# Optimization experiments

Measured on AMD Instinct MI355X. Metric: run time of the kernel, lower is better.

## Reference

```python
import jax, jax.numpy as jnp
import numpy as np


def _forward(x, wc, we, Wb1, bb1, Wb2, bb2, Wr1, br1, Wr2, br2,
             Wq1, bq1, Wq2, bq2, Wq3, bq3, Wo1, bo1, Wo2, bo2, Wo3, bo3, scale):
    bs, c, h, w = x.shape
    Hs, Ws = scale * h, scale * w
    fh = (jnp.arange(Hs, dtype=jnp.float32) + 0.5) / scale
    fw = (jnp.arange(Ws, dtype=jnp.float32) + 0.5) / scale
    coor_h = fh - jnp.floor(fh + 0.001) - 0.5  # [Hs] fractional phase
    coor_w = fw - jnp.floor(fw + 0.001) - 0.5  # [Ws]
    ones_hw = jnp.ones((Hs, Ws), jnp.float32)
    meta = jnp.stack([ones_hw, ones_hw / scale,
                      jnp.broadcast_to(coor_h[:, None], (Hs, Ws)),
                      jnp.broadcast_to(coor_w[None, :], (Hs, Ws))], 0)  # [4,Hs,Ws]
    chan_mean = x.mean(axis=(0, 2, 3))  # [c]
    chan_scale = jnp.concatenate([chan_mean[:, None], jnp.ones((c, 3), jnp.float32)], axis=1)  # [c,4]
    inp = meta[None] * chan_scale[:, :, None, None]  # [c,4,Hs,Ws]

    # body: 1x1x1 Conv3d over spectral-channel axis c
    lin = lambda W, b, t: jnp.einsum('oc,cfhw->ofhw', W, t) + b[:, None, None, None]
    emb = jax.nn.relu(lin(Wb2, bb2, jax.nn.relu(lin(Wb1, bb1, inp))))  # [c,4,Hs,Ws]

    # offset head: Conv2d 1x1 with batch = c, features = 4 -> 2
    lin2 = lambda W, b, t: jnp.einsum('of,cfhw->cohw', W, t) + b[None, :, None, None]
    off = lin2(Wo3, bo3, jax.nn.relu(lin2(Wo2, bo2, jax.nn.relu(lin2(Wo1, bo1, emb)))))  # [c,2,Hs,Ws]

    # routing_1: Conv3d over c -> 1 channel, sigmoid
    r = jax.nn.sigmoid(lin(Wr2, br2, jax.nn.relu(lin(Wr1, br1, emb))))[0]  # [4,Hs,Ws]
    # routing_2: Conv2d 1x1 over the 4 meta-features -> E experts
    lin3 = lambda W, b, t: jnp.einsum('of,fhw->ohw', W, t) + b[:, None, None]
    rw = jax.nn.sigmoid(lin3(Wq3, bq3, jax.nn.relu(lin3(Wq2, bq2, jax.nn.relu(lin3(Wq1, bq1, r))))))  # [E,Hs,Ws]

    # per-channel offset grid_sample (bilinear, zeros padding, align_corners=True)
    px0 = fw - 0.5  # [Ws] base source x coord
    py0 = fh - 0.5  # [Hs]

    def sample(img, offx, offy):  # img [bs,h,w]; off* [Hs,Ws]
        px = px0[None, :] + offx
        py = py0[:, None] + offy
        x0 = jnp.floor(px); y0 = jnp.floor(py)
        wx = px - x0; wy = py - y0
        x0i = x0.astype(jnp.int32); y0i = y0.astype(jnp.int32)
        def g(yi, xi):
            v = ((xi >= 0) & (xi <= w - 1) & (yi >= 0) & (yi <= h - 1)).astype(img.dtype)
            return img[:, jnp.clip(yi, 0, h - 1), jnp.clip(xi, 0, w - 1)] * v[None]
        return (g(y0i, x0i) * ((1 - wy) * (1 - wx))[None]
                + g(y0i, x0i + 1) * ((1 - wy) * wx)[None]
                + g(y0i + 1, x0i) * (wy * (1 - wx))[None]
                + g(y0i + 1, x0i + 1) * (wy * wx)[None])

    fea0 = jax.vmap(lambda xi, oi: sample(xi, oi[0], oi[1]),
                    in_axes=(1, 0), out_axes=1)(x, off)  # [bs,c,Hs,Ws]

    # per-pixel expert-mixed compress/expand: (sum_e r_e Wc_e) f then (sum_e r_e We_e)
    mid = jnp.einsum('ehw,ekc,bchw->bkhw', rw, wc, fea0)   # [bs,c//8,Hs,Ws]
    out = jnp.einsum('ehw,eck,bkhw->bchw', rw, we, mid)    # [bs,c,Hs,Ws]
    return out + fea0


def setup_inputs() -> dict:
    key = jax.random.key(0)
    ks = jax.random.split(key, 32)
    bs, c, h, w = 4, 64, 64, 64
    E, k = 4, c // 8
    s = 0.05
    d = {
        'x': jax.random.normal(ks[0], (bs, c, h, w), jnp.float32),
        'wc': jax.random.normal(ks[1], (E, k, c), jnp.float32) * s,
        'we': jax.random.normal(ks[2], (E, c, k), jnp.float32) * s,
        'Wb1': jax.random.normal(ks[3], (c, c), jnp.float32) * s,
        'bb1': jax.random.normal(ks[4], (c,), jnp.float32) * s,
        'Wb2': jax.random.normal(ks[5], (c, c), jnp.float32) * s,
        'bb2': jax.random.normal(ks[6], (c,), jnp.float32) * s,
        'Wr1': jax.random.normal(ks[7], (64, c), jnp.float32) * s,
        'br1': jax.random.normal(ks[8], (64,), jnp.float32) * s,
        'Wr2': jax.random.normal(ks[9], (1, 64), jnp.float32) * s,
        'br2': jax.random.normal(ks[10], (1,), jnp.float32) * s,
        'Wq1': jax.random.normal(ks[11], (64, 4), jnp.float32) * s,
        'bq1': jax.random.normal(ks[12], (64,), jnp.float32) * s,
        'Wq2': jax.random.normal(ks[13], (64, 64), jnp.float32) * s,
        'bq2': jax.random.normal(ks[14], (64,), jnp.float32) * s,
        'Wq3': jax.random.normal(ks[15], (E, 64), jnp.float32) * s,
        'bq3': jax.random.normal(ks[16], (E,), jnp.float32) * s,
        'Wo1': jax.random.normal(ks[17], (64, 4), jnp.float32) * s,
        'bo1': jax.random.normal(ks[18], (64,), jnp.float32) * s,
        'Wo2': jax.random.normal(ks[19], (64, 64), jnp.float32) * s,
        'bo2': jax.random.normal(ks[20], (64,), jnp.float32) * s,
        'Wo3': jax.random.normal(ks[21], (2, 64), jnp.float32) * s,
        'bo3': jax.random.normal(ks[22], (2,), jnp.float32) * s,
        'scale': 4,
    }
    return d


def reference(x, wc, we, Wb1, bb1, Wb2, bb2, Wr1, br1, Wr2, br2,
              Wq1, bq1, Wq2, bq2, Wq3, bq3, Wo1, bo1, Wo2, bo2, Wo3, bo3, scale):
    return _forward(x, wc, we, Wb1, bb1, Wb2, bb2, Wr1, br1, Wr2, br2,
                    Wq1, bq1, Wq2, bq2, Wq3, bq3, Wo1, bo1, Wo2, bo2, Wo3, bo3, int(scale))
```

## Files before the change

kernel.cpp:

```cpp
#include <hip/hip_runtime.h>


__device__ __forceinline__ float relu_(float v){ return fmaxf(v, 0.f); }
__device__ __forceinline__ float sigm_(float v){ return 1.f/(1.f + __expf(-v)); }

__global__ void k_mean(const float* __restrict__ x, float* __restrict__ ws) {
  const int ch = blockIdx.x, b = blockIdx.y, t = threadIdx.x;
  const float4* p = reinterpret_cast<const float4*>(x + (size_t)(b*64 + ch)*4096);
  float4 v0 = p[t], v1 = p[t+256], v2 = p[t+512], v3 = p[t+768];
  float s = ((v0.x+v0.y)+(v0.z+v0.w)) + ((v1.x+v1.y)+(v1.z+v1.w))
          + ((v2.x+v2.y)+(v2.z+v2.w)) + ((v3.x+v3.y)+(v3.z+v3.w));
  __shared__ float red[256];
  red[t] = s; __syncthreads();
  for (int off = 128; off > 0; off >>= 1) {
    if (t < off) red[t] += red[t + off];
    __syncthreads();
  }
  if (t == 0) ws[18496 + b*64 + ch] = red[0];
}

__launch_bounds__(256)
__global__ void k_phase(const float* __restrict__ wc, const float* __restrict__ we,
    const float* __restrict__ Wb1, const float* __restrict__ bb1,
    const float* __restrict__ Wb2, const float* __restrict__ bb2,
    const float* __restrict__ Wr1, const float* __restrict__ br1,
    const float* __restrict__ Wr2, const float* __restrict__ br2,
    const float* __restrict__ Wq1, const float* __restrict__ bq1,
    const float* __restrict__ Wq2, const float* __restrict__ bq2,
    const float* __restrict__ Wq3, const float* __restrict__ bq3,
    const float* __restrict__ Wo1, const float* __restrict__ bo1,
    const float* __restrict__ Wo2, const float* __restrict__ bo2,
    const float* __restrict__ Wo3, const float* __restrict__ bo3,
    float* __restrict__ ws)
{
  const int p = blockIdx.x, pi = p >> 2, pj = p & 3;
  const int t = threadIdx.x;
  const float chv = 0.25f*pi - 0.375f, cwv = 0.25f*pj - 0.375f;

  __shared__ float WbL1[64*66];
  __shared__ float WbL2[64*66];
  __shared__ float WrL1[64*66];
  __shared__ float WqL2[64*66];
  __shared__ __align__(16) float Wo2L[4096];
  __shared__ __align__(16) float Wo1L[256];
  __shared__ __align__(16) float wcL[2048];
  __shared__ __align__(16) float weL[2048];
  __shared__ float Wo3L[128];
  __shared__ float Wq1L[256], Wq3L[256];
  __shared__ float Wr2L[64];
  __shared__ float bb1L[64], bb2L[64], br1L[64], bq1L[64], bq2L[64];
  __shared__ float bo1L[64], bo2L[64];

  __shared__ float meanL[64];
  __shared__ __align__(16) float t1L[64][4];
  __shared__ __align__(16) float embL[64][4];
  __shared__ __align__(16) float rpL[64][4];
  __shared__ float r4[4];
  __shared__ float q1L[64], q2L[64];
  __shared__ float rwL[4];
  __shared__ float oxL[64][4], oyL[64][4];

  {
    const float* srcs[4] = {Wb1, Wb2, Wr1, Wq2};
    float* dsts[4] = {WbL1, WbL2, WrL1, WqL2};
    for (int m = 0; m < 4; ++m) {
      const float4* W4 = reinterpret_cast<const float4*>(srcs[m]);
      float* WL = dsts[m];
      for (int v = t; v < 1024; v += 256) {
        float4 d = W4[v];
        const int r = v >> 4, c = (v & 15) << 2;
        float* q = &WL[r*66 + c];
        q[0] = d.x; q[1] = d.y; q[2] = d.z; q[3] = d.w;
      }
    }
    for (int v = t; v < 1024; v += 256)
      reinterpret_cast<float4*>(Wo2L)[v] = reinterpret_cast<const float4*>(Wo2)[v];
    for (int v = t; v < 512; v += 256) {
      reinterpret_cast<float4*>(wcL)[v] = reinterpret_cast<const float4*>(wc)[v];
      reinterpret_cast<float4*>(weL)[v] = reinterpret_cast<const float4*>(we)[v];
    }
    if (t < 64) {
      reinterpret_cast<float4*>(Wo1L)[t] = reinterpret_cast<const float4*>(Wo1)[t];
      reinterpret_cast<float4*>(Wq1L)[t] = reinterpret_cast<const float4*>(Wq1)[t];
      reinterpret_cast<float4*>(Wq3L)[t] = reinterpret_cast<const float4*>(Wq3)[t];
      bb1L[t] = bb1[t]; bb2L[t] = bb2[t]; br1L[t] = br1[t];
      bq1L[t] = bq1[t]; bq2L[t] = bq2[t];
      bo1L[t] = bo1[t]; bo2L[t] = bo2[t];
      Wr2L[t] = Wr2[t];
      const float* wsp = ws + 18496;
      meanL[t] = (wsp[t] + wsp[64+t] + wsp[128+t] + wsp[192+t]) * (1.f/16384.f);
    }
    if (t >= 64 && t < 192) Wo3L[t-64] = Wo3[t-64];
  }
  __syncthreads();

  if (t < 64) {
    float a0 = 0.f, as = 0.f;
    const float* row = &WbL1[t*66];
    #pragma unroll 8
    for (int c = 0; c < 64; ++c) { float w = row[c]; a0 += w*meanL[c]; as += w; }
    float bb = bb1L[t];
    t1L[t][0] = relu_(a0 + bb);
    t1L[t][1] = relu_(0.25f*as + bb);
    t1L[t][2] = relu_(chv*as + bb);
    t1L[t][3] = relu_(cwv*as + bb);
  }
  __syncthreads();
  if (t < 64) {
    float bb = bb2L[t];
    float e0=bb,e1=bb,e2=bb,e3=bb;
    const float* row = &WbL2[t*66];
    #pragma unroll 8
    for (int c = 0; c < 64; ++c) {
      float w = row[c];
      float4 tv = *reinterpret_cast<const float4*>(&t1L[c][0]);
      e0 += w*tv.x; e1 += w*tv.y; e2 += w*tv.z; e3 += w*tv.w;
    }
    embL[t][0]=relu_(e0); embL[t][1]=relu_(e1); embL[t][2]=relu_(e2); embL[t][3]=relu_(e3);
  }
  __syncthreads();
  if (t < 64) {
    float bb = br1L[t];
    float p0=bb,p1=bb,p2=bb,p3=bb;
    const float* row = &WrL1[t*66];
    #pragma unroll 8
    for (int c = 0; c < 64; ++c) {
      float w = row[c];
      float4 ev = *reinterpret_cast<const float4*>(&embL[c][0]);
      p0 += w*ev.x; p1 += w*ev.y; p2 += w*ev.z; p3 += w*ev.w;
    }
    rpL[t][0]=relu_(p0); rpL[t][1]=relu_(p1); rpL[t][2]=relu_(p2); rpL[t][3]=relu_(p3);
  }
  __syncthreads();
  if (t < 4) {
    float acc = br2[0];
    #pragma unroll 8
    for (int c = 0; c < 64; ++c) acc += Wr2L[c]*rpL[c][t];
    r4[t] = sigm_(acc);
  }
  __syncthreads();
  if (t < 64) {
    float acc = bq1L[t];
    #pragma unroll
    for (int f = 0; f < 4; ++f) acc += Wq1L[t*4+f]*r4[f];
    q1L[t] = relu_(acc);
  }
  __syncthreads();
  if (t < 64) {
    float acc = bq2L[t];
    const float* row = &WqL2[t*66];
    #pragma unroll 8
    for (int c = 0; c < 64; ++c) acc += row[c]*q1L[c];
    q2L[t] = relu_(acc);
  }
  __syncthreads();
  if (t < 4) {
    float acc = bq3[t];
    #pragma unroll 8
    for (int c = 0; c < 64; ++c) acc += Wq3L[t*64+c]*q2L[c];
    rwL[t] = sigm_(acc);
  }
  __syncthreads();

  {
    const int ch = t & 63, q = t >> 6;
    const float4 e = *reinterpret_cast<const float4*>(&embL[ch][0]);
    float v1[64];
    #pragma unroll
    for (int o = 0; o < 64; ++o) {
      float4 w = *reinterpret_cast<const float4*>(&Wo1L[o*4]);
      v1[o] = relu_(w.x*e.x + w.y*e.y + w.z*e.z + w.w*e.w + bo1L[o]);
    }
    float ox = 0.f, oy = 0.f;
    for (int o = q*16; o < q*16+16; ++o) {
      float acc = bo2L[o];
      const float4* row = reinterpret_cast<const float4*>(&Wo2L[o*64]);
      #pragma unroll
      for (int k = 0; k < 16; ++k) {
        float4 w = row[k];
        acc += w.x*v1[4*k+0] + w.y*v1[4*k+1] + w.z*v1[4*k+2] + w.w*v1[4*k+3];
      }
      acc = relu_(acc);
      ox += Wo3L[o]*acc;
      oy += Wo3L[64+o]*acc;
    }
    oxL[ch][q] = ox; oyL[ch][q] = oy;
  }
  __syncthreads();

  float* ws_off = ws + 64;
  float* ws_wcT = ws + 2112;
  float* ws_weT = ws + 10304;
  if (t < 64) {
    ws_off[(p*64+t)*2+0] = oxL[t][0]+oxL[t][1]+oxL[t][2]+oxL[t][3] + bo3[0];
    ws_off[(p*64+t)*2+1] = oyL[t][0]+oyL[t][1]+oyL[t][2]+oyL[t][3] + bo3[1];
  }
  const float r0 = rwL[0], r1 = rwL[1], r2 = rwL[2], r3 = rwL[3];
  for (int idx = t; idx < 512; idx += 256) {
    const int ch = idx >> 3, k = idx & 7;
    ws_wcT[p*512 + idx] = r0*wcL[(0*8+k)*64+ch] + r1*wcL[(1*8+k)*64+ch]
                        + r2*wcL[(2*8+k)*64+ch] + r3*wcL[(3*8+k)*64+ch];
    ws_weT[p*512 + idx] = r0*weL[(0*64+ch)*8+k] + r1*weL[(1*64+ch)*8+k]
                        + r2*weL[(2*64+ch)*8+k] + r3*weL[(3*64+ch)*8+k];
  }
}

__launch_bounds__(256, 3)
__global__ void k_main(const float* __restrict__ x, const float* __restrict__ ws,
                       float* __restrict__ out) {
  const int i = blockIdx.x;
  const int b = blockIdx.y;
  const int j = threadIdx.x;
  const int pi = i & 3;
  const int pj = j & 3;

  __shared__ float wcT[4*520];
  __shared__ float weT[4*520];
  __shared__ float offxL[4*68];
  __shared__ int4  rowi[256];

  const float* wsoff = ws + 64;
  const float* wswc  = ws + 2112;
  const float* wswe  = ws + 10304;

  for (int idx = threadIdx.x; idx < 2048; idx += 256) {
    const int ph = idx >> 9, rem = idx & 511;
    wcT[ph*520 + rem] = wswc[(pi*4 + ph)*512 + rem];
    weT[ph*520 + rem] = wswe[(pi*4 + ph)*512 + rem];
  }
  {
    const int ch = threadIdx.x >> 2, ph = threadIdx.x & 3;
    const int p = pi*4 + ph;
    const float ox = wsoff[(p*64 + ch)*2 + 0];
    const float oy = wsoff[(p*64 + ch)*2 + 1];
    offxL[ph*68 + ch] = ox;
    const float py = i*0.25f - 0.375f + oy;
    const float fy = floorf(py);
    const float wy = py - fy;
    const int y0 = (int)fy, y1 = y0 + 1;
    const int y0c = min(max(y0, 0), 63), y1c = min(max(y1, 0), 63);
    const float wy0 = ((unsigned)y0 <= 63u) ? (1.f - wy) : 0.f;
    const float wy1 = ((unsigned)y1 <= 63u) ? wy : 0.f;
    rowi[ch*4 + ph] = make_int4(ch*4096 + y0c*64, ch*4096 + y1c*64,
                                __float_as_int(wy0), __float_as_int(wy1));
  }
  __syncthreads();

  const float* __restrict__ xb = x + (size_t)b*64*4096;
  const float px0 = j*0.25f - 0.375f;

  float fea[64];
  float mid[8] = {0.f,0.f,0.f,0.f,0.f,0.f,0.f,0.f};

  const float4* wc_pj = reinterpret_cast<const float4*>(&wcT[pj*520]);
  const float* offx_pj = &offxL[pj*68];
  const int4* rowi_pj = &rowi[pj];

  #pragma unroll
  for (int ch = 0; ch < 64; ++ch) {
    const int4 ri = rowi_pj[ch*4];
    const float px = px0 + offx_pj[ch];
    const float fx = floorf(px);
    const float wx = px - fx;
    const int x0 = (int)fx, x1 = x0 + 1;
    const int x0c = min(max(x0, 0), 63), x1c = min(max(x1, 0), 63);
    const float wx0 = ((unsigned)x0 <= 63u) ? (1.f - wx) : 0.f;
    const float wx1 = ((unsigned)x1 <= 63u) ? wx : 0.f;
    const float g00 = xb[ri.x + x0c], g01 = xb[ri.x + x1c];
    const float g10 = xb[ri.y + x0c], g11 = xb[ri.y + x1c];
    const float f0 = g00*wx0 + g01*wx1;
    const float f1 = g10*wx0 + g11*wx1;
    const float fv = f0*__int_as_float(ri.z) + f1*__int_as_float(ri.w);
    fea[ch] = fv;
    const float4 wa = wc_pj[ch*2], wb = wc_pj[ch*2+1];
    mid[0] += wa.x*fv; mid[1] += wa.y*fv; mid[2] += wa.z*fv; mid[3] += wa.w*fv;
    mid[4] += wb.x*fv; mid[5] += wb.y*fv; mid[6] += wb.z*fv; mid[7] += wb.w*fv;
  }

  const float4* we_pj = reinterpret_cast<const float4*>(&weT[pj*520]);
  float* op = out + (size_t)(b*64)*65536 + i*256 + j;
  #pragma unroll
  for (int ch = 0; ch < 64; ++ch) {
    const float4 wa = we_pj[ch*2], wb = we_pj[ch*2+1];
    float acc = fea[ch];
    acc += wa.x*mid[0] + wa.y*mid[1] + wa.z*mid[2] + wa.w*mid[3];
    acc += wb.x*mid[4] + wb.y*mid[5] + wb.z*mid[6] + wb.w*mid[7];
    op[ch*65536] = acc;
  }
}

extern "C" void kernel_launch(void* const* d_in, const int* in_sizes, int n_in,
                              void* d_out, int out_size, void* d_ws, size_t ws_size,
                              hipStream_t stream) {
  const float* x   = (const float*)d_in[0];
  const float* wc  = (const float*)d_in[1];
  const float* we  = (const float*)d_in[2];
  const float* Wb1 = (const float*)d_in[3];
  const float* bb1 = (const float*)d_in[4];
  const float* Wb2 = (const float*)d_in[5];
  const float* bb2 = (const float*)d_in[6];
  const float* Wr1 = (const float*)d_in[7];
  const float* br1 = (const float*)d_in[8];
  const float* Wr2 = (const float*)d_in[9];
  const float* br2 = (const float*)d_in[10];
  const float* Wq1 = (const float*)d_in[11];
  const float* bq1 = (const float*)d_in[12];
  const float* Wq2 = (const float*)d_in[13];
  const float* bq2 = (const float*)d_in[14];
  const float* Wq3 = (const float*)d_in[15];
  const float* bq3 = (const float*)d_in[16];
  const float* Wo1 = (const float*)d_in[17];
  const float* bo1 = (const float*)d_in[18];
  const float* Wo2 = (const float*)d_in[19];
  const float* bo2 = (const float*)d_in[20];
  const float* Wo3 = (const float*)d_in[21];
  const float* bo3 = (const float*)d_in[22];
  float* ws  = (float*)d_ws;
  float* out = (float*)d_out;

  k_mean<<<dim3(64, 4), 256, 0, stream>>>(x, ws);
  k_phase<<<16, 256, 0, stream>>>(wc, we, Wb1, bb1, Wb2, bb2, Wr1, br1, Wr2, br2,
                                  Wq1, bq1, Wq2, bq2, Wq3, bq3,
                                  Wo1, bo1, Wo2, bo2, Wo3, bo3, ws);
  k_main<<<dim3(256, 4), 256, 0, stream>>>(x, ws, out);
}
```

Before: 163.6 us.

## Remap main kernel so each wavefront owns one phase and reads precomputed tables

The phase kernel now precomputes per-(phase, channel) x-offset parameters, packed interleaved wc/we mixing weights, and full per-row y-index/weight tables into workspace. The main kernel drops its shared-memory staging and barrier, assigns one column phase per wavefront so mixing weights and offsets are wave-uniform scalar loads, and raises launch bounds occupancy to 4. This removes per-block LDS setup and redundant y-coordinate math, but writes output with a stride-4 interleaved column pattern and adds a large y-table in global memory.

New measurement: 197.7 us. 20.8% more time.

```diff
diff --git a/kernel.cpp b/kernel.cpp
--- a/kernel.cpp
+++ b/kernel.cpp
@@ -16,7 +16,7 @@
     if (t < off) red[t] += red[t + off];
     __syncthreads();
   }
-  if (t == 0) ws[18496 + b*64 + ch] = red[0];
+  if (t == 0) ws[b*64 + ch] = red[0];
 }
 
 __launch_bounds__(256)
@@ -59,6 +59,7 @@
   __shared__ float q1L[64], q2L[64];
   __shared__ float rwL[4];
   __shared__ float oxL[64][4], oyL[64][4];
+  __shared__ float oxF[64], oyF[64];
 
   {
     const float* srcs[4] = {Wb1, Wb2, Wr1, Wq2};
@@ -87,7 +88,7 @@
       bq1L[t] = bq1[t]; bq2L[t] = bq2[t];
       bo1L[t] = bo1[t]; bo2L[t] = bo2[t];
       Wr2L[t] = Wr2[t];
-      const float* wsp = ws + 18496;
+      const float* wsp = ws;
       meanL[t] = (wsp[t] + wsp[64+t] + wsp[128+t] + wsp[192+t]) * (1.f/16384.f);
     }
     if (t >= 64 && t < 192) Wo3L[t-64] = Wo3[t-64];
@@ -187,105 +188,113 @@
     oxL[ch][q] = ox; oyL[ch][q] = oy;
   }
   __syncthreads();
-
-  float* ws_off = ws + 64;
-  float* ws_wcT = ws + 2112;
-  float* ws_weT = ws + 10304;
-  if (t < 64) {
-    ws_off[(p*64+t)*2+0] = oxL[t][0]+oxL[t][1]+oxL[t][2]+oxL[t][3] + bo3[0];
-    ws_off[(p*64+t)*2+1] = oyL[t][0]+oyL[t][1]+oyL[t][2]+oyL[t][3] + bo3[1];
-  }
-  const float r0 = rwL[0], r1 = rwL[1], r2 = rwL[2], r3 = rwL[3];
-  for (int idx = t; idx < 512; idx += 256) {
-    const int ch = idx >> 3, k = idx & 7;
-    ws_wcT[p*512 + idx] = r0*wcL[(0*8+k)*64+ch] + r1*wcL[(1*8+k)*64+ch]
-                        + r2*wcL[(2*8+k)*64+ch] + r3*wcL[(3*8+k)*64+ch];
-    ws_weT[p*512 + idx] = r0*weL[(0*64+ch)*8+k] + r1*weL[(1*64+ch)*8+k]
-                        + r2*weL[(2*64+ch)*8+k] + r3*weL[(3*64+ch)*8+k];
+  if (t < 64) {
+    oxF[t] = oxL[t][0]+oxL[t][1]+oxL[t][2]+oxL[t][3] + bo3[0];
+    oyF[t] = oyL[t][0]+oyL[t][1]+oyL[t][2]+oyL[t][3] + bo3[1];
+  }
+  __syncthreads();
+
+  if (t < 64) {
+    const float B = 0.25f*pj - 0.375f + oxF[t];
+    const float bx = floorf(B);
+    const float wx = B - bx;
+    float4 pr;
+    pr.x = __int_as_float((int)bx);
+    pr.y = 1.f - wx;
+    pr.z = wx;
+    pr.w = 0.f;
+    *reinterpret_cast<float4*>(ws + 256 + (p*64 + t)*4) = pr;
+  }
+
+  {
+    const float r0 = rwL[0], r1 = rwL[1], r2 = rwL[2], r3 = rwL[3];
+    for (int idx = t; idx < 1024; idx += 256) {
+      const int ch = idx >> 4, k = idx & 15;
+      float v;
+      if (k < 8) {
+        v = r0*wcL[(0*8+k)*64+ch] + r1*wcL[(1*8+k)*64+ch]
+          + r2*wcL[(2*8+k)*64+ch] + r3*wcL[(3*8+k)*64+ch];
+      } else {
+        const int kk = k - 8;
+        v = r0*weL[(0*64+ch)*8+kk] + r1*weL[(1*64+ch)*8+kk]
+          + r2*weL[(2*64+ch)*8+kk] + r3*weL[(3*64+ch)*8+kk];
+      }
+      ws[4352 + (p*64+ch)*16 + k] = v;
+    }
+  }
+
+  {
+    const int ch = t & 63, iq = t >> 6;
+    const float oy = oyF[ch];
+    float* dst = ws + 20736 + (p*64 + ch)*1024 + iq*256;
+    for (int n = 0; n < 64; ++n) {
+      const int i = iq*64 + n;
+      const float py = i*0.25f - 0.375f + oy;
+      const float fy = floorf(py);
+      const float wy = py - fy;
+      const int y0 = (int)fy, y1 = y0 + 1;
+      const int y0c = min(max(y0, 0), 63), y1c = min(max(y1, 0), 63);
+      const float wy0 = ((unsigned)y0 <= 63u) ? (1.f - wy) : 0.f;
+      const float wy1 = ((unsigned)y1 <= 63u) ? wy : 0.f;
+      float4 yi;
+      yi.x = __int_as_float(ch*4096 + y0c*64);
+      yi.y = __int_as_float(ch*4096 + y1c*64);
+      yi.z = wy0; yi.w = wy1;
+      reinterpret_cast<float4*>(dst)[n] = yi;
+    }
   }
 }
 
-__launch_bounds__(256, 3)
+__launch_bounds__(256, 4)
 __global__ void k_main(const float* __restrict__ x, const float* __restrict__ ws,
                        float* __restrict__ out) {
   const int i = blockIdx.x;
   const int b = blockIdx.y;
-  const int j = threadIdx.x;
-  const int pi = i & 3;
-  const int pj = j & 3;
-
-  __shared__ float wcT[4*520];
-  __shared__ float weT[4*520];
-  __shared__ float offxL[4*68];
-  __shared__ int4  rowi[256];
-
-  const float* wsoff = ws + 64;
-  const float* wswc  = ws + 2112;
-  const float* wswe  = ws + 10304;
-
-  for (int idx = threadIdx.x; idx < 2048; idx += 256) {
-    const int ph = idx >> 9, rem = idx & 511;
-    wcT[ph*520 + rem] = wswc[(pi*4 + ph)*512 + rem];
-    weT[ph*520 + rem] = wswe[(pi*4 + ph)*512 + rem];
-  }
-  {
-    const int ch = threadIdx.x >> 2, ph = threadIdx.x & 3;
-    const int p = pi*4 + ph;
-    const float ox = wsoff[(p*64 + ch)*2 + 0];
-    const float oy = wsoff[(p*64 + ch)*2 + 1];
-    offxL[ph*68 + ch] = ox;
-    const float py = i*0.25f - 0.375f + oy;
-    const float fy = floorf(py);
-    const float wy = py - fy;
-    const int y0 = (int)fy, y1 = y0 + 1;
-    const int y0c = min(max(y0, 0), 63), y1c = min(max(y1, 0), 63);
-    const float wy0 = ((unsigned)y0 <= 63u) ? (1.f - wy) : 0.f;
-    const float wy1 = ((unsigned)y1 <= 63u) ? wy : 0.f;
-    rowi[ch*4 + ph] = make_int4(ch*4096 + y0c*64, ch*4096 + y1c*64,
-                                __float_as_int(wy0), __float_as_int(wy1));
-  }
-  __syncthreads();
-
-  const float* __restrict__ xb = x + (size_t)b*64*4096;
-  const float px0 = j*0.25f - 0.375f;
+  const int w = __builtin_amdgcn_readfirstlane((int)(threadIdx.x >> 6));
+  const int l = threadIdx.x & 63;
+  const int p = (i & 3)*4 + w;
+
+  const float* __restrict__ prm = ws + 256   + p*256;
+  const float* __restrict__ wmx = ws + 4352  + p*1024;
+  const float* __restrict__ yif = ws + 20736 + p*65536 + i*4;
+  const float* __restrict__ xb  = x + (size_t)b*262144;
 
   float fea[64];
-  float mid[8] = {0.f,0.f,0.f,0.f,0.f,0.f,0.f,0.f};
-
-  const float4* wc_pj = reinterpret_cast<const float4*>(&wcT[pj*520]);
-  const float* offx_pj = &offxL[pj*68];
-  const int4* rowi_pj = &rowi[pj];
+  float m0=0.f,m1=0.f,m2=0.f,m3=0.f,m4=0.f,m5=0.f,m6=0.f,m7=0.f;
 
   #pragma unroll
   for (int ch = 0; ch < 64; ++ch) {
-    const int4 ri = rowi_pj[ch*4];
-    const float px = px0 + offx_pj[ch];
-    const float fx = floorf(px);
-    const float wx = px - fx;
-    const int x0 = (int)fx, x1 = x0 + 1;
-    const int x0c = min(max(x0, 0), 63), x1c = min(max(x1, 0), 63);
-    const float wx0 = ((unsigned)x0 <= 63u) ? (1.f - wx) : 0.f;
-    const float wx1 = ((unsigned)x1 <= 63u) ? wx : 0.f;
-    const float g00 = xb[ri.x + x0c], g01 = xb[ri.x + x1c];
-    const float g10 = xb[ri.y + x0c], g11 = xb[ri.y + x1c];
-    const float f0 = g00*wx0 + g01*wx1;
-    const float f1 = g10*wx0 + g11*wx1;
-    const float fv = f0*__int_as_float(ri.z) + f1*__int_as_float(ri.w);
+    const float4 pr = *reinterpret_cast<const float4*>(prm + ch*4);
+    const float4 yi = *reinterpret_cast<const float4*>(yif + ch*1024);
+    const float4 wa = *reinterpret_cast<const float4*>(wmx + ch*16);
+    const float4 wb = *reinterpret_cast<const float4*>(wmx + ch*16 + 4);
+    const int x0 = l + __float_as_int(pr.x);
+    const int x1 = x0 + 1;
+    const int x0c = min(max(x0, 0), 63);
+    const int x1c = min(max(x1, 0), 63);
+    const float u0 = ((unsigned)x0 <= 63u) ? pr.y : 0.f;
+    const float u1 = ((unsigned)x1 <= 63u) ? pr.z : 0.f;
+    const int rb0 = __float_as_int(yi.x), rb1 = __float_as_int(yi.y);
+    const float g00 = xb[rb0 + x0c], g01 = xb[rb0 + x1c];
+    const float g10 = xb[rb1 + x0c], g11 = xb[rb1 + x1c];
+    const float f0 = g00*u0 + g01*u1;
+    const float f1 = g10*u0 + g11*u1;
+    const float fv = f0*yi.z + f1*yi.w;
     fea[ch] = fv;
-    const float4 wa = wc_pj[ch*2], wb = wc_pj[ch*2+1];
-    mid[0] += wa.x*fv; mid[1] += wa.y*fv; mid[2] += wa.z*fv; mid[3] += wa.w*fv;
-    mid[4] += wb.x*fv; mid[5] += wb.y*fv; mid[6] += wb.z*fv; mid[7] += wb.w*fv;
-  }
-
-  const float4* we_pj = reinterpret_cast<const float4*>(&weT[pj*520]);
-  float* op = out + (size_t)(b*64)*65536 + i*256 + j;
+    m0 += wa.x*fv; m1 += wa.y*fv; m2 += wa.z*fv; m3 += wa.w*fv;
+    m4 += wb.x*fv; m5 += wb.y*fv; m6 += wb.z*fv; m7 += wb.w*fv;
+  }
+
+  float* __restrict__ ob = out + (size_t)b*4194304;
+  const int joff = i*256 + 4*l + w;
   #pragma unroll
   for (int ch = 0; ch < 64; ++ch) {
-    const float4 wa = we_pj[ch*2], wb = we_pj[ch*2+1];
+    const float4 wa = *reinterpret_cast<const float4*>(wmx + ch*16 + 8);
+    const float4 wb = *reinterpret_cast<const float4*>(wmx + ch*16 + 12);
     float acc = fea[ch];
-    acc += wa.x*mid[0] + wa.y*mid[1] + wa.z*mid[2] + wa.w*mid[3];
-    acc += wb.x*mid[4] + wb.y*mid[5] + wb.z*mid[6] + wb.w*mid[7];
-    op[ch*65536] = acc;
+    acc += wa.x*m0 + wa.y*m1 + wa.z*m2 + wa.w*m3;
+    acc += wb.x*m4 + wb.y*m5 + wb.z*m6 + wb.w*m7;
+    ob[joff + ch*65536] = acc;
   }
 }
 
```
